# Kernel tuning notes

Hardware: AMD Instinct MI355X
Metric: run time of the kernel (lower is better)

## Reference

```python
import jax, jax.numpy as jnp
import numpy as np

B, NP, NG = 4, 8192, 8192

def setup_inputs() -> dict:
    key = jax.random.key(0)
    k1, k2, k3 = jax.random.split(key, 3)
    pr_pts = jax.random.normal(k1, (B, NP, 3), dtype=jnp.float32)
    gt_pts = jax.random.normal(k2, (B, NG, 3), dtype=jnp.float32)
    gt_valid = jax.random.randint(k3, (B, NG), 0, 2) > 0
    return {"pr_pts": pr_pts, "gt_pts": gt_pts, "gt_valid": gt_valid}

def _sq_dists(a, b):
    # a: [B,N,3], b: [B,M,3] -> squared pairwise distances [B,N,M]
    a2 = jnp.sum(a * a, -1)  # [B,N]
    b2 = jnp.sum(b * b, -1)  # [B,M]
    ab = jnp.einsum('bnd,bmd->bnm', a, b)
    return a2[:, :, None] + b2[:, None, :] - 2.0 * ab

def reference(pr_pts, gt_pts, gt_valid):
    # Bidirectional Chamfer distance with gt validity mask.
    d2 = _sq_dists(pr_pts, gt_pts)  # [B,Np,Ng]
    # accuracy: for each predicted point, min squared dist to a VALID gt point
    d2_masked = jnp.where(gt_valid[:, None, :], d2, jnp.inf)
    acc_b = jnp.mean(jnp.min(d2_masked, axis=-1), axis=-1)  # [B]
    # completeness: for each valid gt point, min squared dist to any pred point
    min_over_pr = jnp.min(d2, axis=1)  # [B,Ng]
    valid_f = gt_valid.astype(min_over_pr.dtype)
    com_b = jnp.sum(min_over_pr * valid_f, axis=-1) / jnp.maximum(jnp.sum(valid_f, axis=-1), 1.0)
    loss_acc = jnp.mean(acc_b)
    loss_com = jnp.mean(com_b)
    loss_cd = loss_acc + loss_com
    # Sum((loss_acc,None),(loss_com,None),(loss_cd,None)) with scalar losses -> acc+com+cd
    return loss_acc + loss_com + loss_cd
```

## Files before the change

kernel.cpp:

```cpp
#include <hip/hip_runtime.h>

#define BB 4
#define NN 8192

typedef _Float16 f16;
typedef _Float16 f16x8 __attribute__((ext_vector_type(8)));
typedef float f32x16 __attribute__((ext_vector_type(16)));

#define SZ_PACK (BB * NN * 16)
#define OFF_PART_BYTES (4 * SZ_PACK * 2)
#define OFF_RES_BYTES (OFF_PART_BYTES + 16 * NN * 4)

__global__ __launch_bounds__(256) void k_init(
    const float* __restrict__ pr, const float* __restrict__ gt,
    const int* __restrict__ valid,
    f16* __restrict__ APR, f16* __restrict__ BGT,
    f16* __restrict__ AGT, f16* __restrict__ BPR,
    float* __restrict__ res) {
  int i = blockIdx.x * 256 + threadIdx.x;
  if (blockIdx.x == 0 && threadIdx.x < 16) res[threadIdx.x] = 0.0f;
  if (i >= BB * NN) return;
  float px = pr[3 * i], py = pr[3 * i + 1], pz = pr[3 * i + 2];
  float gx = gt[3 * i], gy = gt[3 * i + 1], gz = gt[3 * i + 2];
  int vld = valid[i] != 0;

  f16 phx = (f16)px, phy = (f16)py, phz = (f16)pz;
  f16 plx = (f16)(px - (float)phx), ply = (f16)(py - (float)phy), plz = (f16)(pz - (float)phz);
  float p2 = px * px + py * py + pz * pz;
  f16 p2h = (f16)p2, p2l = (f16)(p2 - (float)p2h);

  f16 ghx = (f16)gx, ghy = (f16)gy, ghz = (f16)gz;
  f16 glx = (f16)(gx - (float)ghx), gly = (f16)(gy - (float)ghy), glz = (f16)(gz - (float)ghz);
  float g2 = gx * gx + gy * gy + gz * gz;
  f16 g2h = (f16)g2, g2l = (f16)(g2 - (float)g2h);
  f16 g2hm = vld ? g2h : (f16)32768.0f;
  f16 g2lm = vld ? g2l : (f16)0.0f;

  const f16 one = (f16)1.0f, zero = (f16)0.0f;
  union Rec { f16 h[16]; uint4 u[2]; };

  Rec ra;
  ra.h[0] = (f16)(-2.f * (float)phx); ra.h[1] = (f16)(-2.f * (float)phy); ra.h[2] = (f16)(-2.f * (float)phz);
  ra.h[3] = ra.h[0]; ra.h[4] = ra.h[1]; ra.h[5] = ra.h[2];
  ra.h[6] = (f16)(-2.f * (float)plx); ra.h[7] = (f16)(-2.f * (float)ply); ra.h[8] = (f16)(-2.f * (float)plz);
  ra.h[9] = p2h; ra.h[10] = p2l; ra.h[11] = one; ra.h[12] = one;
  ra.h[13] = zero; ra.h[14] = zero; ra.h[15] = zero;
  ((uint4*)APR)[2 * i] = ra.u[0]; ((uint4*)APR)[2 * i + 1] = ra.u[1];

  Rec rb;
  rb.h[0] = phx; rb.h[1] = phy; rb.h[2] = phz;
  rb.h[3] = plx; rb.h[4] = ply; rb.h[5] = plz;
  rb.h[6] = phx; rb.h[7] = phy; rb.h[8] = phz;
  rb.h[9] = one; rb.h[10] = one; rb.h[11] = p2h; rb.h[12] = p2l;
  rb.h[13] = zero; rb.h[14] = zero; rb.h[15] = zero;
  ((uint4*)BPR)[2 * i] = rb.u[0]; ((uint4*)BPR)[2 * i + 1] = rb.u[1];

  Rec rc;
  rc.h[0] = (f16)(-2.f * (float)ghx); rc.h[1] = (f16)(-2.f * (float)ghy); rc.h[2] = (f16)(-2.f * (float)ghz);
  rc.h[3] = rc.h[0]; rc.h[4] = rc.h[1]; rc.h[5] = rc.h[2];
  rc.h[6] = (f16)(-2.f * (float)glx); rc.h[7] = (f16)(-2.f * (float)gly); rc.h[8] = (f16)(-2.f * (float)glz);
  rc.h[9] = g2h; rc.h[10] = g2l; rc.h[11] = one; rc.h[12] = one;
  rc.h[13] = zero; rc.h[14] = zero; rc.h[15] = zero;
  ((uint4*)AGT)[2 * i] = rc.u[0]; ((uint4*)AGT)[2 * i + 1] = rc.u[1];

  Rec rd;
  rd.h[0] = ghx; rd.h[1] = ghy; rd.h[2] = ghz;
  rd.h[3] = glx; rd.h[4] = gly; rd.h[5] = glz;
  rd.h[6] = ghx; rd.h[7] = ghy; rd.h[8] = ghz;
  rd.h[9] = one; rd.h[10] = one; rd.h[11] = g2hm; rd.h[12] = g2lm;
  rd.h[13] = zero; rd.h[14] = zero; rd.h[15] = zero;
  ((uint4*)BGT)[2 * i] = rd.u[0]; ((uint4*)BGT)[2 * i + 1] = rd.u[1];
}

__global__ __launch_bounds__(256, 2) void k_dist(
    const f16* __restrict__ APR, const f16* __restrict__ BGT,
    const f16* __restrict__ AGT, const f16* __restrict__ BPR,
    float* __restrict__ partial) {
  __shared__ f16 lds[2 * 1024 * 8];
  int id = blockIdx.x;
  int rowwg = id & 31;
  int half  = (id >> 5) & 1;
  int b     = (id >> 6) & 3;
  int p     = id >> 8;
  const f16* A  = p ? AGT : APR;
  const f16* Bv = p ? BPR : BGT;
  int tid = threadIdx.x;
  int wave = tid >> 6, lane = tid & 63;
  int nn = lane & 31, q = lane >> 5;

  const f16* Ab = A + ((size_t)b * NN + rowwg * 256 + wave * 64 + nn) * 16 + q * 8;
  f16x8 af0 = *(const f16x8*)Ab;
  f16x8 af1 = *(const f16x8*)(Ab + 32 * 16);

  f32x16 zc = {};
  f32x16 m0, m1;
#pragma unroll
  for (int i = 0; i < 16; ++i) { m0[i] = 1e38f; m1[i] = 1e38f; }

  const uint4* gsrc = (const uint4*)(Bv + ((size_t)b * NN + half * 4096) * 16);
  uint4* ldsu = (uint4*)lds;
  const f16x8* lf = (const f16x8*)lds;

  for (int chunk = 0; chunk < 4; ++chunk) {
    const uint4* src = gsrc + (size_t)chunk * 2048;
#pragma unroll
    for (int k = 0; k < 8; ++k) {
      int u = tid + 256 * k;
      ldsu[(u & 1) * 1024 + (u >> 1)] = src[u];
    }
    __syncthreads();
    for (int t = 0; t < 32; t += 2) {
      f16x8 b0 = lf[q * 1024 + t * 32 + nn];
      f16x8 b1 = lf[q * 1024 + (t + 1) * 32 + nn];
      f32x16 d00 = __builtin_amdgcn_mfma_f32_32x32x16_f16(af0, b0, zc, 0, 0, 0);
      f32x16 d01 = __builtin_amdgcn_mfma_f32_32x32x16_f16(af0, b1, zc, 0, 0, 0);
#pragma unroll
      for (int i = 0; i < 16; ++i) m0[i] = fminf(fminf(d00[i], d01[i]), m0[i]);
      f32x16 d10 = __builtin_amdgcn_mfma_f32_32x32x16_f16(af1, b0, zc, 0, 0, 0);
      f32x16 d11 = __builtin_amdgcn_mfma_f32_32x32x16_f16(af1, b1, zc, 0, 0, 0);
#pragma unroll
      for (int i = 0; i < 16; ++i) m1[i] = fminf(fminf(d10[i], d11[i]), m1[i]);
    }
    __syncthreads();
  }

#pragma unroll
  for (int i = 0; i < 16; ++i) {
    float v0 = m0[i], v1 = m1[i];
    v0 = fminf(v0, __shfl_xor(v0, 1, 64));
    v1 = fminf(v1, __shfl_xor(v1, 1, 64));
    v0 = fminf(v0, __shfl_xor(v0, 2, 64));
    v1 = fminf(v1, __shfl_xor(v1, 2, 64));
    v0 = fminf(v0, __shfl_xor(v0, 4, 64));
    v1 = fminf(v1, __shfl_xor(v1, 4, 64));
    v0 = fminf(v0, __shfl_xor(v0, 8, 64));
    v1 = fminf(v1, __shfl_xor(v1, 8, 64));
    v0 = fminf(v0, __shfl_xor(v0, 16, 64));
    v1 = fminf(v1, __shfl_xor(v1, 16, 64));
    m0[i] = fmaxf(v0, 0.0f);
    m1[i] = fmaxf(v1, 0.0f);
  }

  float* pb = partial + (((size_t)(p * 4 + b) * 2 + half) * NN) + rowwg * 256 + wave * 64;
#pragma unroll
  for (int reg = 0; reg < 16; ++reg) {
    int rit = (reg & 3) + 8 * (reg >> 2) + 4 * q;
    if ((lane & 31) == reg) {
      pb[rit] = m0[reg];
      pb[32 + rit] = m1[reg];
    }
  }
}

__global__ __launch_bounds__(256) void k_red(
    const float* __restrict__ partial, const int* __restrict__ valid,
    float* __restrict__ res, float* __restrict__ out) {
  int g = blockIdx.x >> 3, seg = blockIdx.x & 7;
  int pp = g >> 2, bb = g & 3;
  int tid = threadIdx.x;
  const float* pb = partial + (size_t)g * 2 * NN;

  float sum = 0.0f, cnt = 0.0f;
#pragma unroll
  for (int k = 0; k < 4; ++k) {
    int r = seg * 1024 + tid + 256 * k;
    float v = fminf(pb[r], pb[NN + r]);
    if (pp == 0) {
      sum += v;
    } else {
      int vld = valid[bb * NN + r] != 0;
      sum += vld ? v : 0.0f;
      cnt += vld ? 1.0f : 0.0f;
    }
  }
  __shared__ float r1[256], r2[256];
  r1[tid] = sum; r2[tid] = cnt;
  __syncthreads();
  for (int off = 128; off > 0; off >>= 1) {
    if (tid < off) { r1[tid] += r1[tid + off]; r2[tid] += r2[tid + off]; }
    __syncthreads();
  }
  if (tid == 0) {
    if (pp == 0) {
      atomicAdd(&res[bb], r1[0]);
    } else {
      atomicAdd(&res[4 + bb], r1[0]);
      atomicAdd(&res[8 + bb], r2[0]);
    }
    __threadfence();
    int done = atomicAdd((int*)&res[12], 1);
    if (done == 63) {
      float a = 0.f, c = 0.f;
      for (int B2 = 0; B2 < 4; ++B2) {
        float tA = atomicAdd(&res[B2], 0.0f);
        float tC = atomicAdd(&res[4 + B2], 0.0f);
        float tN = atomicAdd(&res[8 + B2], 0.0f);
        a += tA / (float)NN;
        c += tC / fmaxf(tN, 1.0f);
      }
      out[0] = 0.5f * (a + c);
    }
  }
}

extern "C" void kernel_launch(void* const* d_in, const int* in_sizes, int n_in,
                              void* d_out, int out_size, void* d_ws, size_t ws_size,
                              hipStream_t stream) {
  const float* pr    = (const float*)d_in[0];
  const float* gt    = (const float*)d_in[1];
  const int*   valid = (const int*)d_in[2];

  f16* base = (f16*)d_ws;
  f16* APR = base;
  f16* BGT = base + SZ_PACK;
  f16* AGT = base + 2 * SZ_PACK;
  f16* BPR = base + 3 * SZ_PACK;
  float* partial = (float*)((char*)d_ws + OFF_PART_BYTES);
  float* res     = (float*)((char*)d_ws + OFF_RES_BYTES);

  k_init<<<(BB * NN) / 256, 256, 0, stream>>>(pr, gt, valid, APR, BGT, AGT, BPR, res);
  k_dist<<<512, 256, 0, stream>>>(APR, BGT, AGT, BPR, partial);
  k_red<<<64, 256, 0, stream>>>(partial, valid, res, (float*)d_out);
}
```

Baseline: 91.94 us.

## Fuse reduction into distance kernel, drop column split, prefetch B chunks via registers

Each distance block now covers the full set of 8192 columns instead of half, so the partial-min buffer and the separate reduction kernel go away. Per-row minima are summed, masked by validity and combined with atomics directly in the distance kernel. The next B chunk is prefetched into registers while MFMAs run on the current chunk, and the chunk size is doubled. The grid halves to 256 blocks at one block per CU, which may lower occupancy and lengthen each block's serial work.

```diff
diff --git a/kernel.cpp b/kernel.cpp
--- a/kernel.cpp
+++ b/kernel.cpp
@@ -2,14 +2,14 @@
 
 #define BB 4
 #define NN 8192
+#define CHUNK 2048
 
 typedef _Float16 f16;
 typedef _Float16 f16x8 __attribute__((ext_vector_type(8)));
 typedef float f32x16 __attribute__((ext_vector_type(16)));
 
 #define SZ_PACK (BB * NN * 16)
-#define OFF_PART_BYTES (4 * SZ_PACK * 2)
-#define OFF_RES_BYTES (OFF_PART_BYTES + 16 * NN * 4)
+#define OFF_RES_BYTES (4 * SZ_PACK * 2)
 
 __global__ __launch_bounds__(256) void k_init(
     const float* __restrict__ pr, const float* __restrict__ gt,
@@ -72,16 +72,16 @@
   ((uint4*)BGT)[2 * i] = rd.u[0]; ((uint4*)BGT)[2 * i + 1] = rd.u[1];
 }
 
-__global__ __launch_bounds__(256, 2) void k_dist(
+__global__ __launch_bounds__(256, 1) void k_dist(
     const f16* __restrict__ APR, const f16* __restrict__ BGT,
     const f16* __restrict__ AGT, const f16* __restrict__ BPR,
-    float* __restrict__ partial) {
-  __shared__ f16 lds[2 * 1024 * 8];
+    const int* __restrict__ valid,
+    float* __restrict__ res, float* __restrict__ out) {
+  __shared__ f16 lds[2 * CHUNK * 8];
   int id = blockIdx.x;
   int rowwg = id & 31;
-  int half  = (id >> 5) & 1;
-  int b     = (id >> 6) & 3;
-  int p     = id >> 8;
+  int b     = (id >> 5) & 3;
+  int p     = id >> 7;
   const f16* A  = p ? AGT : APR;
   const f16* Bv = p ? BPR : BGT;
   int tid = threadIdx.x;
@@ -97,21 +97,29 @@
 #pragma unroll
   for (int i = 0; i < 16; ++i) { m0[i] = 1e38f; m1[i] = 1e38f; }
 
-  const uint4* gsrc = (const uint4*)(Bv + ((size_t)b * NN + half * 4096) * 16);
+  const uint4* gsrc = (const uint4*)(Bv + (size_t)b * NN * 16);
   uint4* ldsu = (uint4*)lds;
   const f16x8* lf = (const f16x8*)lds;
 
+  uint4 stage[16];
+#pragma unroll
+  for (int k = 0; k < 16; ++k) stage[k] = gsrc[tid + 256 * k];
+
   for (int chunk = 0; chunk < 4; ++chunk) {
-    const uint4* src = gsrc + (size_t)chunk * 2048;
-#pragma unroll
-    for (int k = 0; k < 8; ++k) {
+#pragma unroll
+    for (int k = 0; k < 16; ++k) {
       int u = tid + 256 * k;
-      ldsu[(u & 1) * 1024 + (u >> 1)] = src[u];
+      ldsu[(u & 1) * CHUNK + (u >> 1)] = stage[k];
     }
     __syncthreads();
-    for (int t = 0; t < 32; t += 2) {
-      f16x8 b0 = lf[q * 1024 + t * 32 + nn];
-      f16x8 b1 = lf[q * 1024 + (t + 1) * 32 + nn];
+    if (chunk < 3) {
+      const uint4* src = gsrc + (size_t)(chunk + 1) * (CHUNK * 2);
+#pragma unroll
+      for (int k = 0; k < 16; ++k) stage[k] = src[tid + 256 * k];
+    }
+    for (int t = 0; t < CHUNK / 32; t += 2) {
+      f16x8 b0 = lf[q * CHUNK + t * 32 + nn];
+      f16x8 b1 = lf[q * CHUNK + (t + 1) * 32 + nn];
       f32x16 d00 = __builtin_amdgcn_mfma_f32_32x32x16_f16(af0, b0, zc, 0, 0, 0);
       f32x16 d01 = __builtin_amdgcn_mfma_f32_32x32x16_f16(af0, b1, zc, 0, 0, 0);
 #pragma unroll
@@ -141,55 +149,38 @@
     m1[i] = fmaxf(v1, 0.0f);
   }
 
-  float* pb = partial + (((size_t)(p * 4 + b) * 2 + half) * NN) + rowwg * 256 + wave * 64;
-#pragma unroll
-  for (int reg = 0; reg < 16; ++reg) {
-    int rit = (reg & 3) + 8 * (reg >> 2) + 4 * q;
-    if ((lane & 31) == reg) {
-      pb[rit] = m0[reg];
-      pb[32 + rit] = m1[reg];
-    }
-  }
-}
-
-__global__ __launch_bounds__(256) void k_red(
-    const float* __restrict__ partial, const int* __restrict__ valid,
-    float* __restrict__ res, float* __restrict__ out) {
-  int g = blockIdx.x >> 3, seg = blockIdx.x & 7;
-  int pp = g >> 2, bb = g & 3;
-  int tid = threadIdx.x;
-  const float* pb = partial + (size_t)g * 2 * NN;
-
-  float sum = 0.0f, cnt = 0.0f;
-#pragma unroll
-  for (int k = 0; k < 4; ++k) {
-    int r = seg * 1024 + tid + 256 * k;
-    float v = fminf(pb[r], pb[NN + r]);
-    if (pp == 0) {
-      sum += v;
+  int rowbase = b * NN + rowwg * 256 + wave * 64;
+  float sA = 0.0f, sC = 0.0f, sN = 0.0f;
+  if (p == 0) {
+#pragma unroll
+    for (int reg = 0; reg < 16; ++reg) sA += m0[reg] + m1[reg];
+  } else {
+#pragma unroll
+    for (int reg = 0; reg < 16; ++reg) {
+      int r0 = (reg & 3) + 8 * (reg >> 2) + 4 * q;
+      int v0 = valid[rowbase + r0] != 0;
+      int v1 = valid[rowbase + r0 + 32] != 0;
+      sC += v0 ? m0[reg] : 0.0f;
+      sC += v1 ? m1[reg] : 0.0f;
+      sN += (float)(v0 + v1);
+    }
+  }
+
+  float* redbuf = (float*)lds;
+  if (nn == 0) { redbuf[wave * 2 + q] = (p == 0) ? sA : sC; redbuf[8 + wave * 2 + q] = sN; }
+  __syncthreads();
+  if (tid == 0) {
+    float t1 = 0.0f, t2 = 0.0f;
+    for (int k = 0; k < 8; ++k) { t1 += redbuf[k]; t2 += redbuf[8 + k]; }
+    if (p == 0) {
+      atomicAdd(&res[b], t1);
     } else {
-      int vld = valid[bb * NN + r] != 0;
-      sum += vld ? v : 0.0f;
-      cnt += vld ? 1.0f : 0.0f;
-    }
-  }
-  __shared__ float r1[256], r2[256];
-  r1[tid] = sum; r2[tid] = cnt;
-  __syncthreads();
-  for (int off = 128; off > 0; off >>= 1) {
-    if (tid < off) { r1[tid] += r1[tid + off]; r2[tid] += r2[tid + off]; }
-    __syncthreads();
-  }
-  if (tid == 0) {
-    if (pp == 0) {
-      atomicAdd(&res[bb], r1[0]);
-    } else {
-      atomicAdd(&res[4 + bb], r1[0]);
-      atomicAdd(&res[8 + bb], r2[0]);
+      atomicAdd(&res[4 + b], t1);
+      atomicAdd(&res[8 + b], t2);
     }
     __threadfence();
     int done = atomicAdd((int*)&res[12], 1);
-    if (done == 63) {
+    if (done == 255) {
       float a = 0.f, c = 0.f;
       for (int B2 = 0; B2 < 4; ++B2) {
         float tA = atomicAdd(&res[B2], 0.0f);
@@ -215,10 +206,8 @@
   f16* BGT = base + SZ_PACK;
   f16* AGT = base + 2 * SZ_PACK;
   f16* BPR = base + 3 * SZ_PACK;
-  float* partial = (float*)((char*)d_ws + OFF_PART_BYTES);
-  float* res     = (float*)((char*)d_ws + OFF_RES_BYTES);
+  float* res = (float*)((char*)d_ws + OFF_RES_BYTES);
 
   k_init<<<(BB * NN) / 256, 256, 0, stream>>>(pr, gt, valid, APR, BGT, AGT, BPR, res);
-  k_dist<<<512, 256, 0, stream>>>(APR, BGT, AGT, BPR, partial);
-  k_red<<<64, 256, 0, stream>>>(partial, valid, res, (float*)d_out);
+  k_dist<<<256, 256, 0, stream>>>(APR, BGT, AGT, BPR, valid, res, (float*)d_out);
 }
```

New measurement: 124.7 us. 35.6% more time.
